# Kernel tuning notes

Measured on AMD Instinct MI355X. Metric: run time of the kernel, lower is better.

The kernel has to match this reference:

```python
import jax, jax.numpy as jnp
import numpy as np

B, T, E, WIN, OC, VOCAB = 256, 2048, 128, 5, 128, 50000


def setup_inputs() -> dict:
    key = jax.random.key(0)
    k1, k2, k3, k4, k5, k6 = jax.random.split(key, 6)
    return {
        "x": jax.random.randint(k1, (B, T), 0, VOCAB + 1, dtype=jnp.int32),
        "emb_table": jax.random.normal(k2, (VOCAB + 1, E), dtype=jnp.float32),
        "att_w": jax.random.normal(k3, (WIN, E), dtype=jnp.float32) * 0.05,
        "att_b": jax.random.normal(k4, (1,), dtype=jnp.float32),
        "cnn_w": jax.random.normal(k5, (OC, E), dtype=jnp.float32) * 0.05,
        "cnn_b": jax.random.normal(k6, (OC,), dtype=jnp.float32),
    }


def reference(x, emb_table, att_w, att_b, cnn_w, cnn_b):
    win = att_w.shape[0]
    pad = (win - 1) // 2
    embed = emb_table[x]                                   # [B, T, E]
    x_pad = jnp.pad(embed, ((0, 0), (pad, pad), (0, 0)))
    T_ = embed.shape[1]
    # Sliding-window dot product over full embed dim (the degenerate Conv2d)
    s = jnp.zeros(embed.shape[:2], dtype=embed.dtype)      # [B, T]
    for k in range(win):
        s = s + jnp.einsum('bte,e->bt', x_pad[:, k:k + T_, :], att_w[k])
    scores = jax.nn.sigmoid(s + att_b[0])                  # [B, T]
    gated = embed * scores[:, :, None]                     # [B, T, E]
    feat = jnp.tanh(jnp.einsum('bte,oe->bto', gated, cnn_w) + cnn_b)  # [B, T, OC]
    out = jnp.max(feat, axis=1)                            # [B, OC] (maxpool over seq)
    return out[:, :, None, None]                           # [B, OC, 1, 1]
```

## Files before the change

### kernel.cpp

```cpp
#include <hip/hip_runtime.h>
#include <hip/hip_bf16.h>
#include <math.h>

#define B_   256
#define T_   2048
#define E_   128
#define WIN_ 5
#define PAD_ 2
#define OC_  128
#define VOCAB_MAX 50000
#define VOCAB1 50001
#define TT   64
#define REAL_ROWS (TT + WIN_ - 1)
#define ROWS 80
#define ASTR 136
#define VROWS 64
#define BT   256

typedef __attribute__((ext_vector_type(8))) short short8;
typedef __attribute__((ext_vector_type(4))) float floatx4;
typedef __attribute__((ext_vector_type(4))) unsigned uintx4;

static __device__ __forceinline__ short f2bf(float f) {
    union { __hip_bfloat16 h; short s; } u;
    u.h = __float2bfloat16(f);
    return u.s;
}

__device__ __forceinline__ void atomicMaxFloat(float* addr, float v) {
    if (v >= 0.0f) atomicMax((int*)addr, __float_as_int(v));
    else           atomicMin((unsigned int*)addr, __float_as_uint(v));
}

__launch_bounds__(256, 4)
__global__ void build_tables(const float* __restrict__ emb,
                             const float* __restrict__ cnn_w,
                             const float* __restrict__ att_w,
                             short* __restrict__ D,
                             float* __restrict__ r,
                             float* __restrict__ out) {
    __shared__ __align__(16) short sh_a[VROWS * ASTR];
    __shared__ __align__(16) short sh_d[VROWS * ASTR];

    const int tid  = threadIdx.x;
    const int lane = tid & 63;
    const int w    = tid >> 6;
    const int l15  = lane & 15;
    const int quad = lane >> 4;
    const int v0   = blockIdx.x * VROWS;

    if (blockIdx.x < (B_ * OC_) / 256)
        out[blockIdx.x * 256 + tid] = -INFINITY;

    #pragma unroll
    for (int t = 0; t < 8; t++) {
        int i   = t * 256 + tid;
        int row = i >> 5, c4 = i & 31;
        int vr  = v0 + row; if (vr > VOCAB_MAX) vr = VOCAB_MAX;
        float4 v = *(const float4*)(emb + (size_t)vr * E_ + c4 * 4);
        short4 o; o.x = f2bf(v.x); o.y = f2bf(v.y); o.z = f2bf(v.z); o.w = f2bf(v.w);
        *(short4*)(&sh_a[row * ASTR + c4 * 4]) = o;
    }

    short8 Bf[2][4];
    #pragma unroll
    for (int j = 0; j < 2; j++)
        #pragma unroll
        for (int ks = 0; ks < 4; ks++) {
            const float4* p = (const float4*)(cnn_w + (size_t)(w * 32 + j * 16 + l15) * E_ + ks * 32 + quad * 8);
            float4 p0 = p[0], p1 = p[1];
            Bf[j][ks] = (short8){ f2bf(p0.x), f2bf(p0.y), f2bf(p0.z), f2bf(p0.w),
                                  f2bf(p1.x), f2bf(p1.y), f2bf(p1.z), f2bf(p1.w) };
        }

    short8 Ba[4];
    #pragma unroll
    for (int ks = 0; ks < 4; ks++) {
        short8 v = (short8){0,0,0,0,0,0,0,0};
        if (l15 < WIN_) {
            const float4* p = (const float4*)(att_w + (size_t)l15 * E_ + ks * 32 + quad * 8);
            float4 p0 = p[0], p1 = p[1];
            v = (short8){ f2bf(p0.x), f2bf(p0.y), f2bf(p0.z), f2bf(p0.w),
                          f2bf(p1.x), f2bf(p1.y), f2bf(p1.z), f2bf(p1.w) };
        }
        Ba[ks] = v;
    }
    __syncthreads();

    #pragma unroll
    for (int mt = 0; mt < 4; mt++) {
        short8 a[4];
        #pragma unroll
        for (int ks = 0; ks < 4; ks++)
            a[ks] = *(const short8*)(&sh_a[(mt * 16 + l15) * ASTR + ks * 32 + quad * 8]);
        #pragma unroll
        for (int j = 0; j < 2; j++) {
            floatx4 acc = (floatx4){0.f, 0.f, 0.f, 0.f};
            #pragma unroll
            for (int ks = 0; ks < 4; ks++)
                acc = __builtin_amdgcn_mfma_f32_16x16x32_bf16(a[ks], Bf[j][ks], acc, 0, 0, 0);
            #pragma unroll
            for (int rr = 0; rr < 4; rr++)
                sh_d[(mt * 16 + quad * 4 + rr) * ASTR + w * 32 + j * 16 + l15] = f2bf(acc[rr]);
        }
    }

    {
        short8 a[4];
        #pragma unroll
        for (int ks = 0; ks < 4; ks++)
            a[ks] = *(const short8*)(&sh_a[(w * 16 + l15) * ASTR + ks * 32 + quad * 8]);
        floatx4 acc = (floatx4){0.f, 0.f, 0.f, 0.f};
        #pragma unroll
        for (int ks = 0; ks < 4; ks++)
            acc = __builtin_amdgcn_mfma_f32_16x16x32_bf16(a[ks], Ba[ks], acc, 0, 0, 0);
        if (l15 < 8) {
            #pragma unroll
            for (int rr = 0; rr < 4; rr++) {
                int v = v0 + w * 16 + quad * 4 + rr;
                if (v <= VOCAB_MAX) r[(size_t)v * 8 + l15] = acc[rr];
            }
        }
    }
    __syncthreads();

    #pragma unroll
    for (int st = 0; st < 4; st++) {
        int i   = st * 256 + tid;
        int row = i >> 4, c = i & 15;
        int v   = v0 + row;
        if (v <= VOCAB_MAX)
            *(short8*)(D + (size_t)v * E_ + c * 8) =
                *(const short8*)(&sh_d[row * ASTR + c * 8]);
    }
}

__launch_bounds__(256, 6)
__global__ void score_max(const int* __restrict__ x,
                          const short* __restrict__ D,
                          const float* __restrict__ r,
                          const float* __restrict__ att_b_p,
                          const float* __restrict__ cnn_b,
                          float* __restrict__ out) {
    __shared__ int   sh_x[BT + 4];
    __shared__ float sh_rt[WIN_][BT + 8];
    __shared__ float sh_sc[BT];
    __shared__ float sh_red[4][128];

    const int tid  = threadIdx.x;
    const int lane = tid & 63;
    const int w    = tid >> 6;
    const int b    = blockIdx.y;
    const int t0   = blockIdx.x * BT;
    const int l15  = lane & 15;
    const int grp  = lane >> 4;

    for (int i = tid; i < BT + 4; i += 256) {
        int t = t0 + i - PAD_;
        int v = (t >= 0 && t < T_) ? x[b * T_ + t] : -1;
        sh_x[i] = v;
        float4 r03 = make_float4(0.f, 0.f, 0.f, 0.f);
        float  r4  = 0.f;
        if (v >= 0) {
            r03 = *(const float4*)(r + (size_t)v * 8);
            r4  = r[(size_t)v * 8 + 4];
        }
        sh_rt[0][i] = r03.x; sh_rt[1][i] = r03.y; sh_rt[2][i] = r03.z;
        sh_rt[3][i] = r03.w; sh_rt[4][i] = r4;
    }
    __syncthreads();

    const int base_t = w * 64;

    uintx4 uA[8];
    #pragma unroll
    for (int j = 0; j < 8; j++) {
        int tok = base_t + j * 4 + grp;
        int v   = sh_x[tok + PAD_];
        uA[j]   = *(const uintx4*)(D + (size_t)v * E_ + l15 * 8);
    }

    {
        const float attb = att_b_p[0];
        float s = attb;
        #pragma unroll
        for (int k = 0; k < WIN_; k++) s += sh_rt[k][tid + k];
        sh_sc[tid] = 1.0f / (1.0f + __expf(-s));
    }
    __syncthreads();

    float mm[8];
    #pragma unroll
    for (int c = 0; c < 8; c++) mm[c] = -INFINITY;

    #pragma unroll
    for (int batch = 0; batch < 2; batch++) {
        uintx4 uB[8];
        if (batch < 1) {
            const int nstart = base_t + 32;
            #pragma unroll
            for (int j = 0; j < 8; j++) {
                int tok = nstart + j * 4 + grp;
                int v   = sh_x[tok + PAD_];
                uB[j]   = *(const uintx4*)(D + (size_t)v * E_ + l15 * 8);
            }
        }

        const int start = base_t + batch * 32;
        float sc8[8];
        #pragma unroll
        for (int j = 0; j < 8; j++) sc8[j] = sh_sc[start + j * 4 + grp];

        #pragma unroll
        for (int j = 0; j < 8; j++) {
            #pragma unroll
            for (int q = 0; q < 4; q++) {
                float lo = __uint_as_float(uA[j][q] << 16);
                float hi = __uint_as_float(uA[j][q] & 0xFFFF0000u);
                mm[q * 2]     = fmaxf(mm[q * 2],     sc8[j] * lo);
                mm[q * 2 + 1] = fmaxf(mm[q * 2 + 1], sc8[j] * hi);
            }
        }

        #pragma unroll
        for (int j = 0; j < 8; j++) uA[j] = uB[j];
    }

    #pragma unroll
    for (int c = 0; c < 8; c++) {
        mm[c] = fmaxf(mm[c], __shfl_xor(mm[c], 16));
        mm[c] = fmaxf(mm[c], __shfl_xor(mm[c], 32));
    }
    if (lane < 16) {
        #pragma unroll
        for (int c = 0; c < 8; c++) sh_red[w][l15 * 8 + c] = mm[c];
    }
    __syncthreads();
    if (tid < 128) {
        float m = fmaxf(fmaxf(sh_red[0][tid], sh_red[1][tid]),
                        fmaxf(sh_red[2][tid], sh_red[3][tid]));
        atomicMaxFloat(&out[b * OC_ + tid], tanhf(m + cnn_b[tid]));
    }
}

__global__ void prep_small(const float* __restrict__ cnn_w, const float* __restrict__ att_w,
                           short* __restrict__ wsw, short* __restrict__ wsatt) {
    int i = blockIdx.x * 256 + threadIdx.x;
    if (i < OC_ * E_)  wsw[i]   = f2bf(cnn_w[i]);
    if (i < WIN_ * E_) wsatt[i] = f2bf(att_w[i]);
}

__launch_bounds__(256, 4)
__global__ void fallback_main(const int* __restrict__ x,
                              const float* __restrict__ emb,
                              const float* __restrict__ att_b_p,
                              const short* __restrict__ wsw,
                              const short* __restrict__ wsatt,
                              const float* __restrict__ cnn_b,
                              float* __restrict__ out) {
    __shared__ short sh_a[ROWS * ASTR];
    __shared__ short sh_att[16 * ASTR];
    __shared__ float sh_r[ROWS * 8];
    __shared__ float sh_score[TT];
    __shared__ int   sh_idx[8 * ROWS];

    const int tid  = threadIdx.x;
    const int lane = tid & 63;
    const int w    = tid >> 6;
    const int b    = blockIdx.y;
    const int t0   = blockIdx.x * (8 * TT);
    const int l15  = lane & 15;
    const int quad = lane >> 4;
    const int rbase = tid >> 4;
    const int c     = tid & 15;

    for (int i = tid; i < 8 * ROWS; i += 256) {
        int tile = i / ROWS, row = i - tile * ROWS;
        int t = t0 + tile * TT + row - PAD_;
        sh_idx[i] = (row < REAL_ROWS && t >= 0 && t < T_) ? x[b * T_ + t] : -1;
    }
    {
        int o = tid >> 4, cc = tid & 15;
        short8 v = (short8){0,0,0,0,0,0,0,0};
        if (o < WIN_) v = *(const short8*)(wsatt + o * E_ + cc * 8);
        *(short8*)(&sh_att[o * ASTR + cc * 8]) = v;
    }
    short8 Bf[2][4];
    #pragma unroll
    for (int j = 0; j < 2; j++)
        #pragma unroll
        for (int ks = 0; ks < 4; ks++)
            Bf[j][ks] = *(const short8*)(wsw + (size_t)(w * 32 + j * 16 + l15) * E_ + ks * 32 + quad * 8);
    __syncthreads();

    short8 g[5];
    #pragma unroll
    for (int k = 0; k < 5; k++) {
        int idx = sh_idx[rbase + 16 * k];
        short8 v = (short8){0,0,0,0,0,0,0,0};
        if (idx >= 0) {
            const float4* p = (const float4*)(emb + (size_t)idx * E_ + c * 8);
            float4 p0 = p[0], p1 = p[1];
            v = (short8){ f2bf(p0.x), f2bf(p0.y), f2bf(p0.z), f2bf(p0.w),
                          f2bf(p1.x), f2bf(p1.y), f2bf(p1.z), f2bf(p1.w) };
        }
        g[k] = v;
    }
    #pragma unroll
    for (int k = 0; k < 5; k++)
        *(short8*)(&sh_a[(rbase + 16 * k) * ASTR + c * 8]) = g[k];
    __syncthreads();

    const float attb = att_b_p[0];
    float mm[2] = { -INFINITY, -INFINITY };

    for (int it = 0; it < 8; it++) {
        for (int mt = w; mt < 5; mt += 4) {
            floatx4 acc = (floatx4){0.f, 0.f, 0.f, 0.f};
            #pragma unroll
            for (int ks = 0; ks < 4; ks++) {
                short8 a  = *(const short8*)(&sh_a[(mt * 16 + l15) * ASTR + ks * 32 + quad * 8]);
                short8 bs = *(const short8*)(&sh_att[l15 * ASTR + ks * 32 + quad * 8]);
                acc = __builtin_amdgcn_mfma_f32_16x16x32_bf16(a, bs, acc, 0, 0, 0);
            }
            if (l15 < 8) {
                #pragma unroll
                for (int r = 0; r < 4; r++)
                    sh_r[(mt * 16 + quad * 4 + r) * 8 + l15] = acc[r];
            }
        }
        __syncthreads();

        if (it + 1 < 8) {
            const int* idxp = &sh_idx[(it + 1) * ROWS];
            #pragma unroll
            for (int k = 0; k < 5; k++) {
                int idx = idxp[rbase + 16 * k];
                short8 v = (short8){0,0,0,0,0,0,0,0};
                if (idx >= 0) {
                    const float4* p = (const float4*)(emb + (size_t)idx * E_ + c * 8);
                    float4 p0 = p[0], p1 = p[1];
                    v = (short8){ f2bf(p0.x), f2bf(p0.y), f2bf(p0.z), f2bf(p0.w),
                                  f2bf(p1.x), f2bf(p1.y), f2bf(p1.z), f2bf(p1.w) };
                }
                g[k] = v;
            }
        }

        if (tid < TT) {
            float s = attb;
            #pragma unroll
            for (int k = 0; k < WIN_; k++) s += sh_r[(tid + k) * 8 + k];
            sh_score[tid] = 1.0f / (1.0f + __expf(-s));
        }

        floatx4 acc[4][2];
        #pragma unroll
        for (int i = 0; i < 4; i++)
            #pragma unroll
            for (int j = 0; j < 2; j++) acc[i][j] = (floatx4){0.f, 0.f, 0.f, 0.f};
        #pragma unroll
        for (int ks = 0; ks < 4; ks++) {
            int ko = ks * 32 + quad * 8;
            #pragma unroll
            for (int i = 0; i < 4; i++) {
                short8 ai = *(const short8*)(&sh_a[(PAD_ + i * 16 + l15) * ASTR + ko]);
                acc[i][0] = __builtin_amdgcn_mfma_f32_16x16x32_bf16(ai, Bf[0][ks], acc[i][0], 0, 0, 0);
                acc[i][1] = __builtin_amdgcn_mfma_f32_16x16x32_bf16(ai, Bf[1][ks], acc[i][1], 0, 0, 0);
            }
        }
        __syncthreads();

        #pragma unroll
        for (int i = 0; i < 4; i++) {
            #pragma unroll
            for (int r = 0; r < 4; r++) {
                float sc = sh_score[i * 16 + quad * 4 + r];
                mm[0] = fmaxf(mm[0], sc * acc[i][0][r]);
                mm[1] = fmaxf(mm[1], sc * acc[i][1][r]);
            }
        }

        if (it + 1 < 8) {
            #pragma unroll
            for (int k = 0; k < 5; k++)
                *(short8*)(&sh_a[(rbase + 16 * k) * ASTR + c * 8]) = g[k];
            __syncthreads();
        }
    }

    #pragma unroll
    for (int j = 0; j < 2; j++) {
        float m = mm[j];
        m = fmaxf(m, __shfl_xor(m, 16));
        m = fmaxf(m, __shfl_xor(m, 32));
        if (lane < 16) {
            int o = w * 32 + j * 16 + lane;
            atomicMaxFloat(&out[b * OC_ + o], tanhf(m + cnn_b[o]));
        }
    }
}

extern "C" void kernel_launch(void* const* d_in, const int* in_sizes, int n_in,
                              void* d_out, int out_size, void* d_ws, size_t ws_size,
                              hipStream_t stream) {
    const int*   x     = (const int*)d_in[0];
    const float* emb   = (const float*)d_in[1];
    const float* att_w = (const float*)d_in[2];
    const float* att_b = (const float*)d_in[3];
    const float* cnn_w = (const float*)d_in[4];
    const float* cnn_b = (const float*)d_in[5];
    float* out = (float*)d_out;

    const size_t d_elems = (size_t)VOCAB1 * E_;
    const size_t r_elems = (size_t)VOCAB1 * 8;
    const size_t need = d_elems * 2 + r_elems * 4 + 64;

    if (ws_size >= need) {
        short* Dt = (short*)d_ws;
        float* rt = (float*)(Dt + d_elems);
        build_tables<<<(VOCAB1 + VROWS - 1) / VROWS, 256, 0, stream>>>(emb, cnn_w, att_w, Dt, rt, out);
        dim3 grid(T_ / BT, B_);
        score_max<<<grid, 256, 0, stream>>>(x, Dt, rt, att_b, cnn_b, out);
    } else {
        hipMemsetAsync(d_out, 0xFF, (size_t)B_ * OC_ * sizeof(float), stream);
        short* ws_w   = (short*)d_ws;
        short* ws_att = ws_w + OC_ * E_;
        prep_small<<<16, 256, 0, stream>>>(cnn_w, att_w, ws_w, ws_att);
        dim3 grid(T_ / (8 * TT), B_);
        fallback_main<<<grid, 256, 0, stream>>>(x, emb, att_b, ws_w, ws_att, cnn_b, out);
    }
}
```

Baseline: 112.7 us.

## Quantize per-vocab projected table to int8 with per-row scales

The precomputed vocab-by-channel projection table moves from bf16 to int8, with one absmax scale per vocab row stored separately and folded into the gating score. This halves the bytes gathered per token in the max-pool kernel, and each lane now covers 16 channels from a single 16-byte load. The cost is extra quantization work and a larger fp32 shared buffer in the table build, plus a loss of precision (about 7 bits) in the pre-activation values, which may exceed the tolerance.

```diff
diff --git a/kernel.cpp b/kernel.cpp
--- a/kernel.cpp
+++ b/kernel.cpp
@@ -14,6 +14,7 @@
 #define REAL_ROWS (TT + WIN_ - 1)
 #define ROWS 80
 #define ASTR 136
+#define DSTR 132
 #define VROWS 64
 #define BT   256
 
@@ -32,15 +33,17 @@
     else           atomicMin((unsigned int*)addr, __float_as_uint(v));
 }
 
-__launch_bounds__(256, 4)
+__launch_bounds__(256, 3)
 __global__ void build_tables(const float* __restrict__ emb,
                              const float* __restrict__ cnn_w,
                              const float* __restrict__ att_w,
-                             short* __restrict__ D,
+                             unsigned char* __restrict__ D8,
                              float* __restrict__ r,
+                             float* __restrict__ rs,
                              float* __restrict__ out) {
     __shared__ __align__(16) short sh_a[VROWS * ASTR];
-    __shared__ __align__(16) short sh_d[VROWS * ASTR];
+    __shared__ __align__(16) float sh_df[VROWS * DSTR];
+    __shared__ float sh_inv[VROWS];
 
     const int tid  = threadIdx.x;
     const int lane = tid & 63;
@@ -101,7 +104,7 @@
                 acc = __builtin_amdgcn_mfma_f32_16x16x32_bf16(a[ks], Bf[j][ks], acc, 0, 0, 0);
             #pragma unroll
             for (int rr = 0; rr < 4; rr++)
-                sh_d[(mt * 16 + quad * 4 + rr) * ASTR + w * 32 + j * 16 + l15] = f2bf(acc[rr]);
+                sh_df[(mt * 16 + quad * 4 + rr) * DSTR + w * 32 + j * 16 + l15] = acc[rr];
         }
     }
 
@@ -124,25 +127,58 @@
     }
     __syncthreads();
 
-    #pragma unroll
-    for (int st = 0; st < 4; st++) {
-        int i   = st * 256 + tid;
-        int row = i >> 4, c = i & 15;
-        int v   = v0 + row;
+    {
+        int row = tid >> 2, seg = tid & 3;
+        const float4* p = (const float4*)(&sh_df[row * DSTR + seg * 32]);
+        float m = 0.f;
+        #pragma unroll
+        for (int k = 0; k < 8; k++) {
+            float4 v = p[k];
+            m = fmaxf(m, fmaxf(fmaxf(fabsf(v.x), fabsf(v.y)), fmaxf(fabsf(v.z), fabsf(v.w))));
+        }
+        m = fmaxf(m, __shfl_xor(m, 1));
+        m = fmaxf(m, __shfl_xor(m, 2));
+        if (seg == 0) {
+            sh_inv[row] = (m > 0.f) ? 127.f / m : 0.f;
+            int v = v0 + row;
+            if (v <= VOCAB_MAX) rs[v] = m * (1.f / 127.f);
+        }
+    }
+    __syncthreads();
+
+    #pragma unroll
+    for (int st = 0; st < 2; st++) {
+        int idx = st * 256 + tid;
+        int row = idx >> 3, c8 = idx & 7;
+        float inv = sh_inv[row];
+        const float* p = &sh_df[row * DSTR + c8 * 16];
+        uintx4 outw;
+        #pragma unroll
+        for (int q = 0; q < 4; q++) {
+            unsigned dw = 0;
+            #pragma unroll
+            for (int k = 0; k < 4; k++) {
+                int qi = (int)rintf(p[q * 4 + k] * inv);
+                dw |= ((unsigned)(qi & 0xFF)) << (k * 8);
+            }
+            outw[q] = dw;
+        }
+        int v = v0 + row;
         if (v <= VOCAB_MAX)
-            *(short8*)(D + (size_t)v * E_ + c * 8) =
-                *(const short8*)(&sh_d[row * ASTR + c * 8]);
-    }
-}
-
-__launch_bounds__(256, 6)
+            *(uintx4*)(D8 + (size_t)v * OC_ + c8 * 16) = outw;
+    }
+}
+
+__launch_bounds__(256, 4)
 __global__ void score_max(const int* __restrict__ x,
-                          const short* __restrict__ D,
+                          const unsigned char* __restrict__ D8,
                           const float* __restrict__ r,
+                          const float* __restrict__ rs,
                           const float* __restrict__ att_b_p,
                           const float* __restrict__ cnn_b,
                           float* __restrict__ out) {
     __shared__ int   sh_x[BT + 4];
+    __shared__ float sh_rs[BT + 4];
     __shared__ float sh_rt[WIN_][BT + 8];
     __shared__ float sh_sc[BT];
     __shared__ float sh_red[4][128];
@@ -152,32 +188,34 @@
     const int w    = tid >> 6;
     const int b    = blockIdx.y;
     const int t0   = blockIdx.x * BT;
-    const int l15  = lane & 15;
-    const int grp  = lane >> 4;
+    const int l7   = lane & 7;
+    const int grp8 = lane >> 3;
 
     for (int i = tid; i < BT + 4; i += 256) {
         int t = t0 + i - PAD_;
         int v = (t >= 0 && t < T_) ? x[b * T_ + t] : -1;
         sh_x[i] = v;
         float4 r03 = make_float4(0.f, 0.f, 0.f, 0.f);
-        float  r4  = 0.f;
+        float  r4  = 0.f, rsv = 0.f;
         if (v >= 0) {
             r03 = *(const float4*)(r + (size_t)v * 8);
             r4  = r[(size_t)v * 8 + 4];
+            rsv = rs[v];
         }
         sh_rt[0][i] = r03.x; sh_rt[1][i] = r03.y; sh_rt[2][i] = r03.z;
         sh_rt[3][i] = r03.w; sh_rt[4][i] = r4;
+        sh_rs[i] = rsv;
     }
     __syncthreads();
 
     const int base_t = w * 64;
 
-    uintx4 uA[8];
+    uintx4 u[8];
     #pragma unroll
     for (int j = 0; j < 8; j++) {
-        int tok = base_t + j * 4 + grp;
+        int tok = base_t + j * 8 + grp8;
         int v   = sh_x[tok + PAD_];
-        uA[j]   = *(const uintx4*)(D + (size_t)v * E_ + l15 * 8);
+        u[j]    = *(const uintx4*)(D8 + (size_t)v * OC_ + l7 * 16);
     }
 
     {
@@ -185,55 +223,40 @@
         float s = attb;
         #pragma unroll
         for (int k = 0; k < WIN_; k++) s += sh_rt[k][tid + k];
-        sh_sc[tid] = 1.0f / (1.0f + __expf(-s));
-    }
-    __syncthreads();
-
-    float mm[8];
-    #pragma unroll
-    for (int c = 0; c < 8; c++) mm[c] = -INFINITY;
-
-    #pragma unroll
-    for (int batch = 0; batch < 2; batch++) {
-        uintx4 uB[8];
-        if (batch < 1) {
-            const int nstart = base_t + 32;
-            #pragma unroll
-            for (int j = 0; j < 8; j++) {
-                int tok = nstart + j * 4 + grp;
-                int v   = sh_x[tok + PAD_];
-                uB[j]   = *(const uintx4*)(D + (size_t)v * E_ + l15 * 8);
-            }
-        }
-
-        const int start = base_t + batch * 32;
-        float sc8[8];
-        #pragma unroll
-        for (int j = 0; j < 8; j++) sc8[j] = sh_sc[start + j * 4 + grp];
-
-        #pragma unroll
-        for (int j = 0; j < 8; j++) {
-            #pragma unroll
-            for (int q = 0; q < 4; q++) {
-                float lo = __uint_as_float(uA[j][q] << 16);
-                float hi = __uint_as_float(uA[j][q] & 0xFFFF0000u);
-                mm[q * 2]     = fmaxf(mm[q * 2],     sc8[j] * lo);
-                mm[q * 2 + 1] = fmaxf(mm[q * 2 + 1], sc8[j] * hi);
-            }
-        }
-
-        #pragma unroll
-        for (int j = 0; j < 8; j++) uA[j] = uB[j];
-    }
-
-    #pragma unroll
-    for (int c = 0; c < 8; c++) {
+        sh_sc[tid] = sh_rs[tid + PAD_] / (1.0f + __expf(-s));
+    }
+    __syncthreads();
+
+    float mm[16];
+    #pragma unroll
+    for (int c = 0; c < 16; c++) mm[c] = -INFINITY;
+
+    float sc8[8];
+    #pragma unroll
+    for (int j = 0; j < 8; j++) sc8[j] = sh_sc[base_t + j * 8 + grp8];
+
+    #pragma unroll
+    for (int j = 0; j < 8; j++) {
+        #pragma unroll
+        for (int q = 0; q < 4; q++) {
+            unsigned dw = u[j][q];
+            #pragma unroll
+            for (int k = 0; k < 4; k++) {
+                int val = ((int)dw << (24 - k * 8)) >> 24;
+                mm[q * 4 + k] = fmaxf(mm[q * 4 + k], sc8[j] * (float)val);
+            }
+        }
+    }
+
+    #pragma unroll
+    for (int c = 0; c < 16; c++) {
+        mm[c] = fmaxf(mm[c], __shfl_xor(mm[c], 8));
         mm[c] = fmaxf(mm[c], __shfl_xor(mm[c], 16));
         mm[c] = fmaxf(mm[c], __shfl_xor(mm[c], 32));
     }
-    if (lane < 16) {
-        #pragma unroll
-        for (int c = 0; c < 8; c++) sh_red[w][l15 * 8 + c] = mm[c];
+    if (grp8 == 0) {
+        #pragma unroll
+        for (int c = 0; c < 16; c++) sh_red[w][l7 * 16 + c] = mm[c];
     }
     __syncthreads();
     if (tid < 128) {
@@ -412,16 +435,18 @@
     const float* cnn_b = (const float*)d_in[5];
     float* out = (float*)d_out;
 
-    const size_t d_elems = (size_t)VOCAB1 * E_;
-    const size_t r_elems = (size_t)VOCAB1 * 8;
-    const size_t need = d_elems * 2 + r_elems * 4 + 64;
+    const size_t d8_bytes = (size_t)VOCAB1 * OC_;
+    const size_t r_bytes  = (size_t)VOCAB1 * 8 * 4;
+    const size_t rs_bytes = (size_t)VOCAB1 * 4;
+    const size_t need = d8_bytes + r_bytes + rs_bytes + 64;
 
     if (ws_size >= need) {
-        short* Dt = (short*)d_ws;
-        float* rt = (float*)(Dt + d_elems);
-        build_tables<<<(VOCAB1 + VROWS - 1) / VROWS, 256, 0, stream>>>(emb, cnn_w, att_w, Dt, rt, out);
+        unsigned char* D8 = (unsigned char*)d_ws;
+        float* rt = (float*)(D8 + d8_bytes);
+        float* rsp = (float*)((char*)d_ws + d8_bytes + r_bytes);
+        build_tables<<<(VOCAB1 + VROWS - 1) / VROWS, 256, 0, stream>>>(emb, cnn_w, att_w, D8, rt, rsp, out);
         dim3 grid(T_ / BT, B_);
-        score_max<<<grid, 256, 0, stream>>>(x, Dt, rt, att_b, cnn_b, out);
+        score_max<<<grid, 256, 0, stream>>>(x, D8, rt, rsp, att_b, cnn_b, out);
     } else {
         hipMemsetAsync(d_out, 0xFF, (size_t)B_ * OC_ * sizeof(float), stream);
         short* ws_w   = (short*)d_ws;
```

After: 106.4 us. 5.6% less time.
